# Kernel tuning notes

Measured on AMD Instinct MI355X. Metric: run time of the kernel, lower is better.

Reference implementation:

```python
import jax, jax.numpy as jnp
import numpy as np

B, N, C, H = 2, 4096, 512, 8
D = C // H          # head dim = 64
EPS = 1e-5          # nn.LayerNorm default eps


def _layernorm(x, gamma, beta):
    m = jnp.mean(x, axis=-1, keepdims=True)
    v = jnp.var(x, axis=-1, keepdims=True)
    return (x - m) * jax.lax.rsqrt(v + EPS) * gamma + beta


def setup_inputs() -> dict:
    key = jax.random.key(0)
    k_x, k_w = jax.random.split(key, 2)
    return {
        "x": jax.random.normal(k_x, (B, N, C), dtype=jnp.float32),
        "w_qkv": jax.random.normal(k_w, (C, 3 * C), dtype=jnp.float32) * 0.02,
        "b_qkv": jnp.zeros((3 * C,), dtype=jnp.float32),
        "g_pre": jnp.ones((C,), dtype=jnp.float32),
        "beta_pre": jnp.zeros((C,), dtype=jnp.float32),
        "g_post": jnp.ones((C,), dtype=jnp.float32),
        "beta_post": jnp.zeros((C,), dtype=jnp.float32),
    }


def reference(x, w_qkv, b_qkv, g_pre, beta_pre, g_post, beta_post):
    b, n, c = x.shape
    xn = _layernorm(x, g_pre, beta_pre)                       # pre_norm (x is reassigned in source)
    qkv = (xn @ w_qkv + b_qkv).reshape(b, n, 3, H, D)
    qkv = jnp.transpose(qkv, (2, 0, 3, 1, 4))                 # [3, B, H, N, D]
    q, k, v = qkv[0], qkv[1], qkv[2]
    scale = D ** (-0.5)
    attn = jnp.einsum('bhnd,bhmd->bhnm', q, k) * scale        # [B, H, N, N]
    soft = jax.nn.softmax(attn, axis=-1)
    val = jnp.einsum('bhnm,bhmd->bhnd', soft, v)              # [B, H, N, D]
    val = jnp.transpose(val, (0, 2, 1, 3)).reshape(b, n, c)   # [B, N, C]
    val = _layernorm(val, g_post, beta_post)                  # post_norm
    return xn + val                                            # residual uses pre-normed x (faithful)
```

## Files before the change

### kernel.cpp

```cpp
#include <hip/hip_runtime.h>

#define BB   2
#define NN   4096
#define CC   512
#define HH   8
#define DD   64
#define MR   8192
#define NC3  1536
#define PS   4194304
#define SPLK 1408

typedef __attribute__((ext_vector_type(8))) short short8;
typedef __attribute__((ext_vector_type(4))) short short4v;
typedef __attribute__((ext_vector_type(4))) float floatx4;

#if __has_builtin(__builtin_amdgcn_mfma_f32_16x16x16_bf16_1k)
#define MFMA16(a, b, c) __builtin_amdgcn_mfma_f32_16x16x16_bf16_1k(a, b, c, 0, 0, 0)
#elif __has_builtin(__builtin_amdgcn_mfma_f32_16x16x16_bf16)
#define MFMA16(a, b, c) __builtin_amdgcn_mfma_f32_16x16x16_bf16(a, b, c, 0, 0, 0)
#else
__device__ inline floatx4 mfma16_asm(short4v a, short4v b, floatx4 c) {
  asm volatile("v_mfma_f32_16x16x16_bf16 %0, %1, %2, %0" : "+v"(c) : "v"(a), "v"(b));
  return c;
}
#define MFMA16(a, b, c) mfma16_asm(a, b, c)
#endif

__device__ inline unsigned short f2bf(float f) {
  unsigned int u = __float_as_uint(f);
  u = (u + 0x7fffu + ((u >> 16) & 1u)) >> 16;
  return (unsigned short)u;
}

__device__ inline unsigned int pack_bf2(float a, float b) {
  unsigned int ua = __float_as_uint(a) + 0x8000u;
  unsigned int ub = __float_as_uint(b) + 0x8000u;
  return (ub & 0xffff0000u) | (ua >> 16);
}

__device__ inline short4v pack_bf4(float a, float b, float c, float d) {
  union { unsigned int u[2]; short4v v; } t;
  t.u[0] = pack_bf2(a, b);
  t.u[1] = pack_bf2(c, d);
  return t.v;
}

__device__ inline floatx4 fzero4() { floatx4 z = {0.f, 0.f, 0.f, 0.f}; return z; }

__device__ inline void async_cp16(const void* g, void* l) {
  __builtin_amdgcn_global_load_lds(
      (const __attribute__((address_space(1))) unsigned int*)g,
      (__attribute__((address_space(3))) unsigned int*)l, 16, 0, 0);
}

__global__ __launch_bounds__(256) void convert_w_kernel(
    const float* __restrict__ w, unsigned short* __restrict__ wt) {
  __shared__ short T[64][68];
  int bn = blockIdx.x;
  int bk = blockIdx.y;
  int tid = threadIdx.x;
  for (int p = 0; p < 4; p++) {
    int k = p * 16 + (tid >> 4);
    int n4 = (tid & 15) * 4;
    float4 v = *(const float4*)&w[(size_t)(bk * 64 + k) * NC3 + bn * 64 + n4];
    T[n4 + 0][k] = (short)f2bf(v.x);
    T[n4 + 1][k] = (short)f2bf(v.y);
    T[n4 + 2][k] = (short)f2bf(v.z);
    T[n4 + 3][k] = (short)f2bf(v.w);
  }
  __syncthreads();
  for (int p = 0; p < 2; p++) {
    int n = p * 32 + (tid >> 3);
    int k8 = (tid & 7) * 8;
    uint4 v = *(uint4*)&T[n][k8];
    *(uint4*)&wt[(size_t)(bn * 64 + n) * 512 + bk * 64 + k8] = v;
  }
}

__global__ __launch_bounds__(256) void pre_ln_kernel(
    const float* __restrict__ x, const float* __restrict__ g,
    const float* __restrict__ be, unsigned short* __restrict__ xnb) {
  int wv = threadIdx.x >> 6, lane = threadIdx.x & 63;
  int row = blockIdx.x * 4 + wv;
  const float4* xr = (const float4*)(x + (size_t)row * CC);
  float4 v0 = xr[lane];
  float4 v1 = xr[64 + lane];
  float s  = (v0.x + v0.y) + (v0.z + v0.w) + (v1.x + v1.y) + (v1.z + v1.w);
  float sq = (v0.x * v0.x + v0.y * v0.y) + (v0.z * v0.z + v0.w * v0.w) +
             (v1.x * v1.x + v1.y * v1.y) + (v1.z * v1.z + v1.w * v1.w);
  for (int off = 1; off < 64; off <<= 1) {
    s  += __shfl_xor(s,  off, 64);
    sq += __shfl_xor(sq, off, 64);
  }
  float mean = s * (1.0f / CC);
  float var  = sq * (1.0f / CC) - mean * mean;
  float rstd = rsqrtf(var + 1e-5f);
  const float4* gg = (const float4*)g;
  const float4* bb = (const float4*)be;
  float4 g0 = gg[lane], g1 = gg[64 + lane];
  float4 b0 = bb[lane], b1 = bb[64 + lane];
  float4 o0, o1;
  o0.x = (v0.x - mean) * rstd * g0.x + b0.x;
  o0.y = (v0.y - mean) * rstd * g0.y + b0.y;
  o0.z = (v0.z - mean) * rstd * g0.z + b0.z;
  o0.w = (v0.w - mean) * rstd * g0.w + b0.w;
  o1.x = (v1.x - mean) * rstd * g1.x + b1.x;
  o1.y = (v1.y - mean) * rstd * g1.y + b1.y;
  o1.z = (v1.z - mean) * rstd * g1.z + b1.z;
  o1.w = (v1.w - mean) * rstd * g1.w + b1.w;
  size_t base = (size_t)row * CC;
  uint2 u0, u1;
  u0.x = pack_bf2(o0.x, o0.y); u0.y = pack_bf2(o0.z, o0.w);
  u1.x = pack_bf2(o1.x, o1.y); u1.y = pack_bf2(o1.z, o1.w);
  *(uint2*)&xnb[base + 4 * lane] = u0;
  *(uint2*)&xnb[base + 256 + 4 * lane] = u1;
}

#define QSCALE 0.180336879f

__global__ __launch_bounds__(256) void qkv_gemm_kernel(
    const unsigned short* __restrict__ xnb, const unsigned short* __restrict__ wt,
    const float* __restrict__ bias, unsigned short* __restrict__ qkvb) {
  __shared__ __align__(16) char smem[65536];
  short (*Asb[2])[64];
  short (*Bsb[2])[64];
  Asb[0] = (short (*)[64])smem;
  Bsb[0] = (short (*)[64])(smem + 16384);
  Asb[1] = (short (*)[64])(smem + 32768);
  Bsb[1] = (short (*)[64])(smem + 49152);
  short (*T)[136] = (short (*)[136])smem;

  int tn = blockIdx.x;
  int tm = blockIdx.y;
  int tid = threadIdx.x;
  int wv = tid >> 6, lane = tid & 63;
  int quad = lane >> 4, l16 = lane & 15;
  int wm = wv >> 1, wn = wv & 1;
  int l7 = l16 & 7;

  int kr = lane >> 3;
  int kg = (lane & 7) ^ kr;

  floatx4 acc[4][4];
  for (int i = 0; i < 4; i++) for (int j = 0; j < 4; j++) acc[i][j] = fzero4();

  for (int i = 0; i < 4; i++) {
    int rb = i * 32 + wv * 8;
    async_cp16(&xnb[(size_t)(tm * 128 + rb + kr) * 512 + kg * 8], &Asb[0][rb][0]);
    async_cp16(&wt [(size_t)(tn * 128 + rb + kr) * 512 + kg * 8], &Bsb[0][rb][0]);
  }

  for (int it = 0; it < 8; it++) {
    __syncthreads();
    short (*As)[64] = Asb[it & 1];
    short (*Bs)[64] = Bsb[it & 1];
    if (it < 7) {
      int kn = (it + 1) * 64;
      short (*An)[64] = Asb[(it + 1) & 1];
      short (*Bn)[64] = Bsb[(it + 1) & 1];
      for (int i = 0; i < 4; i++) {
        int rb = i * 32 + wv * 8;
        async_cp16(&xnb[(size_t)(tm * 128 + rb + kr) * 512 + kn + kg * 8], &An[rb][0]);
        async_cp16(&wt [(size_t)(tn * 128 + rb + kr) * 512 + kn + kg * 8], &Bn[rb][0]);
      }
    }
    for (int kk = 0; kk < 2; kk++) {
      short8 a[4], b[4];
      for (int mt = 0; mt < 4; mt++)
        a[mt] = *(const short8*)&As[wm * 64 + mt * 16 + l16][((kk * 4 + quad) ^ l7) * 8];
      for (int nt = 0; nt < 4; nt++)
        b[nt] = *(const short8*)&Bs[wn * 64 + nt * 16 + l16][((kk * 4 + quad) ^ l7) * 8];
      for (int mt = 0; mt < 4; mt++)
        for (int nt = 0; nt < 4; nt++)
          acc[mt][nt] = __builtin_amdgcn_mfma_f32_16x16x32_bf16(a[mt], b[nt], acc[mt][nt], 0, 0, 0);
    }
  }
  __syncthreads();

  int part = tn >> 2;
  int b = tm >> 5;
  int tloc = (tm & 31) * 128;

  if (part < 2) {
    for (int nt = 0; nt < 4; nt++) {
      int coll = wn * 64 + nt * 16 + l16;
      float bv = bias[tn * 128 + coll];
      for (int mt = 0; mt < 4; mt++) {
        int rowb = wm * 64 + mt * 16 + quad * 4;
        for (int r = 0; r < 4; r++) {
          float v = acc[mt][nt][r] + bv;
          if (part == 0) v *= QSCALE;
          T[rowb + r][coll] = (short)f2bf(v);
        }
      }
    }
    __syncthreads();
    int h0 = (tn & 3) * 2;
    for (int it = 0; it < 8; it++) {
      int row = it * 16 + (tid >> 4);
      int l = tid & 15;
      uint4 vv = *(uint4*)&T[row][l * 8];
      int h = h0 + (l >> 3), d = (l & 7) * 8;
      size_t idx = (size_t)part * PS +
                   ((size_t)((b * 8 + h) * 4096 + tloc + row)) * 64 + d;
      *(uint4*)&qkvb[idx] = vv;
    }
  } else {
    for (int nt = 0; nt < 4; nt++) {
      int coll = wn * 64 + nt * 16 + l16;
      float bv = bias[tn * 128 + coll];
      for (int mt = 0; mt < 4; mt++) {
        int rowb = wm * 64 + mt * 16 + quad * 4;
        uint2 w;
        w.x = pack_bf2(acc[mt][nt][0] + bv, acc[mt][nt][1] + bv);
        w.y = pack_bf2(acc[mt][nt][2] + bv, acc[mt][nt][3] + bv);
        *(uint2*)&T[coll][rowb] = w;
      }
    }
    __syncthreads();
    for (int it = 0; it < 8; it++) {
      int vrow = it * 16 + (tid >> 4);
      int l = tid & 15;
      uint4 vv = *(uint4*)&T[vrow][l * 8];
      int gj = tn * 128 + vrow;
      int h = (gj >> 6) & 7, d = gj & 63;
      size_t idx = 2 * (size_t)PS +
                   ((size_t)((b * 8 + h) * 64 + d)) * 4096 + tloc + l * 8;
      *(uint4*)&qkvb[idx] = vv;
    }
  }
}

#define SMEM_ATT (16384 + 32768)

__global__ __launch_bounds__(256, 3) void attn_kernel(
    const unsigned short* __restrict__ qkvb, unsigned short* __restrict__ valp,
    float* __restrict__ lsum) {
  __shared__ __align__(16) char smem[SMEM_ATT];
  short (*Ks)[64]   = (short (*)[64])smem;
  short (*Vt0)[128] = (short (*)[128])(smem + 16384);
  short (*Vt1)[128] = (short (*)[128])(smem + 32768);
  float (*slab)[68] = (float (*)[68])smem;

  int bh = blockIdx.y;
  int qb = blockIdx.x * 128;
  int ksp = blockIdx.z;
  int kts = (ksp < 2) ? 11 : 10;
  int tid = threadIdx.x;
  int wv = tid >> 6, lane = tid & 63, quad = lane >> 4, l16 = lane & 15;
  int l7 = l16 & 7;
  const unsigned short* Qg = qkvb + (size_t)bh * NN * DD;
  const unsigned short* Kg = qkvb + (size_t)PS + (size_t)bh * NN * DD +
                             (size_t)ksp * SPLK * DD;
  const unsigned short* Vg = qkvb + 2 * (size_t)PS + (size_t)bh * DD * NN +
                             (size_t)ksp * SPLK;

  int kr = lane >> 3;
  int kg = (lane & 7) ^ kr;
  int vr = lane >> 4;
  int vgr = (lane & 15) ^ ((wv * 4 + vr) & 15);

  for (int i = 0; i < 4; i++) {
    int rb = i * 32 + wv * 8;
    async_cp16(&Qg[(size_t)(qb + rb + kr) * 64 + kg * 8], &Ks[rb][0]);
  }
  __syncthreads();
  short8 qf[2][2];
  for (int g = 0; g < 2; g++)
    for (int kk = 0; kk < 2; kk++)
      qf[g][kk] = *(const short8*)&Ks[wv * 32 + g * 16 + l16][((kk * 4 + quad) ^ l7) * 8];
  __syncthreads();

  for (int i = 0; i < 4; i++) {
    int rb = i * 32 + wv * 8;
    async_cp16(&Kg[(size_t)(rb + kr) * 64 + kg * 8], &Ks[rb][0]);
  }
  for (int i = 0; i < 4; i++) {
    int rb = i * 16 + wv * 4;
    async_cp16(&Vg[(size_t)(rb + vr) * NN + vgr * 8], &Vt0[rb][0]);
  }

  floatx4 o[2][4];
  for (int g = 0; g < 2; g++) for (int dt = 0; dt < 4; dt++) o[g][dt] = fzero4();
  float ls[2] = {0.0f, 0.0f};

  for (int kt = 0; kt < kts; kt++) {
    __syncthreads();
    short (*Vc)[128] = (kt & 1) ? Vt1 : Vt0;
    short (*Vn)[128] = (kt & 1) ? Vt0 : Vt1;
    if (kt + 1 < kts) {
      int kn = (kt + 1) * 128;
      for (int i = 0; i < 4; i++) {
        int rb = i * 16 + wv * 4;
        async_cp16(&Vg[(size_t)(rb + vr) * NN + kn + vgr * 8], &Vn[rb][0]);
      }
    }

    floatx4 s[2][8];
    for (int nt = 0; nt < 8; nt++) {
      short8 kf0 = *(const short8*)&Ks[nt * 16 + l16][((quad) ^ l7) * 8];
      short8 kf1 = *(const short8*)&Ks[nt * 16 + l16][((4 + quad) ^ l7) * 8];
      floatx4 s0 = fzero4(), s1 = fzero4();
      s0 = __builtin_amdgcn_mfma_f32_16x16x32_bf16(kf0, qf[0][0], s0, 0, 0, 0);
      s0 = __builtin_amdgcn_mfma_f32_16x16x32_bf16(kf1, qf[0][1], s0, 0, 0, 0);
      s1 = __builtin_amdgcn_mfma_f32_16x16x32_bf16(kf0, qf[1][0], s1, 0, 0, 0);
      s1 = __builtin_amdgcn_mfma_f32_16x16x32_bf16(kf1, qf[1][1], s1, 0, 0, 0);
      s[0][nt] = s0;
      s[1][nt] = s1;
    }
    __syncthreads();
    if (kt + 1 < kts) {
      int kn = (kt + 1) * 128;
      for (int i = 0; i < 4; i++) {
        int rb = i * 32 + wv * 8;
        async_cp16(&Kg[(size_t)(kn + rb + kr) * 64 + kg * 8], &Ks[rb][0]);
      }
    }

    for (int nt = 0; nt < 8; nt++) {
      float p00 = __builtin_amdgcn_exp2f(s[0][nt][0]);
      float p01 = __builtin_amdgcn_exp2f(s[0][nt][1]);
      float p02 = __builtin_amdgcn_exp2f(s[0][nt][2]);
      float p03 = __builtin_amdgcn_exp2f(s[0][nt][3]);
      float p10 = __builtin_amdgcn_exp2f(s[1][nt][0]);
      float p11 = __builtin_amdgcn_exp2f(s[1][nt][1]);
      float p12 = __builtin_amdgcn_exp2f(s[1][nt][2]);
      float p13 = __builtin_amdgcn_exp2f(s[1][nt][3]);
      ls[0] += (p00 + p01) + (p02 + p03);
      ls[1] += (p10 + p11) + (p12 + p13);
      short4v pa0 = pack_bf4(p00, p01, p02, p03);
      short4v pa1 = pack_bf4(p10, p11, p12, p13);
      for (int dt = 0; dt < 4; dt++) {
        short4v vb = *(const short4v*)&Vc[dt * 16 + l16]
            [(((nt * 2 + (quad >> 1)) ^ l16) * 8) + (quad & 1) * 4];
        o[0][dt] = MFMA16(vb, pa0, o[0][dt]);
        o[1][dt] = MFMA16(vb, pa1, o[1][dt]);
      }
    }
  }

  for (int g = 0; g < 2; g++) {
    ls[g] += __shfl_xor(ls[g], 16, 64);
    ls[g] += __shfl_xor(ls[g], 32, 64);
  }
  float* lrow = lsum + (size_t)(ksp * 16 + bh) * 4096 + qb;
  if (lane < 16) {
    lrow[wv * 32 + l16] = ls[0];
    lrow[wv * 32 + 16 + l16] = ls[1];
  }

  __syncthreads();
  for (int g = 0; g < 2; g++) {
    int q = wv * 32 + g * 16 + l16;
    for (int dt = 0; dt < 4; dt++)
      for (int r = 0; r < 4; r++)
        slab[q][dt * 16 + quad * 4 + r] = o[g][dt][r];
  }
  __syncthreads();
  int b = bh >> 3, h = bh & 7;
  unsigned short* myval = valp + (size_t)ksp * MR * CC;
  for (int it = 0; it < 4; it++) {
    int row = it * 32 + (tid >> 3);
    int col8 = (tid & 7) * 8;
    float4 a = *(float4*)&slab[row][col8];
    float4 c = *(float4*)&slab[row][col8 + 4];
    uint4 u;
    u.x = pack_bf2(a.x, a.y);  u.y = pack_bf2(a.z, a.w);
    u.z = pack_bf2(c.x, c.y);  u.w = pack_bf2(c.z, c.w);
    *(uint4*)&myval[((size_t)(b * 4096 + qb + row)) * 512 + h * 64 + col8] = u;
  }
}

__global__ __launch_bounds__(256) void post_ln_kernel(
    const unsigned short* __restrict__ valp, const float* __restrict__ lsum,
    const unsigned short* __restrict__ xnb,
    const float* __restrict__ g, const float* __restrict__ be,
    float* __restrict__ out) {
  int wv = threadIdx.x >> 6, lane = threadIdx.x & 63;
  int row = blockIdx.x * 4 + wv;
  int b = row >> 12, q = row & 4095;
  int h = lane >> 3;
  float acc[8];
  for (int j = 0; j < 8; j++) acc[j] = 0.0f;
  float lt = 0.0f;
  for (int sp = 0; sp < 3; sp++) {
    uint4 u = *(const uint4*)&valp[((size_t)sp * MR + row) * CC + lane * 8];
    acc[0] += __uint_as_float(u.x << 16);
    acc[1] += __uint_as_float(u.x & 0xffff0000u);
    acc[2] += __uint_as_float(u.y << 16);
    acc[3] += __uint_as_float(u.y & 0xffff0000u);
    acc[4] += __uint_as_float(u.z << 16);
    acc[5] += __uint_as_float(u.z & 0xffff0000u);
    acc[6] += __uint_as_float(u.w << 16);
    acc[7] += __uint_as_float(u.w & 0xffff0000u);
    lt += lsum[(size_t)(sp * 16 + b * 8 + h) * 4096 + q];
  }
  float inv = 1.0f / lt;
  float s = 0.0f, sq = 0.0f;
  for (int j = 0; j < 8; j++) {
    acc[j] *= inv;
    s += acc[j];
    sq += acc[j] * acc[j];
  }
  for (int off = 1; off < 64; off <<= 1) {
    s  += __shfl_xor(s,  off, 64);
    sq += __shfl_xor(sq, off, 64);
  }
  float mean = s * (1.0f / CC);
  float var  = sq * (1.0f / CC) - mean * mean;
  float rstd = rsqrtf(var + 1e-5f);
  float4 g0 = ((const float4*)g)[lane * 2];
  float4 g1 = ((const float4*)g)[lane * 2 + 1];
  float4 b0 = ((const float4*)be)[lane * 2];
  float4 b1 = ((const float4*)be)[lane * 2 + 1];
  size_t base = (size_t)row * CC + lane * 8;
  uint4 xr = *(const uint4*)&xnb[base];
  float r[8];
  r[0] = __uint_as_float(xr.x << 16);  r[1] = __uint_as_float(xr.x & 0xffff0000u);
  r[2] = __uint_as_float(xr.y << 16);  r[3] = __uint_as_float(xr.y & 0xffff0000u);
  r[4] = __uint_as_float(xr.z << 16);  r[5] = __uint_as_float(xr.z & 0xffff0000u);
  r[6] = __uint_as_float(xr.w << 16);  r[7] = __uint_as_float(xr.w & 0xffff0000u);
  float4 o0, o1;
  o0.x = (acc[0] - mean) * rstd * g0.x + b0.x + r[0];
  o0.y = (acc[1] - mean) * rstd * g0.y + b0.y + r[1];
  o0.z = (acc[2] - mean) * rstd * g0.z + b0.z + r[2];
  o0.w = (acc[3] - mean) * rstd * g0.w + b0.w + r[3];
  o1.x = (acc[4] - mean) * rstd * g1.x + b1.x + r[4];
  o1.y = (acc[5] - mean) * rstd * g1.y + b1.y + r[5];
  o1.z = (acc[6] - mean) * rstd * g1.z + b1.z + r[6];
  o1.w = (acc[7] - mean) * rstd * g1.w + b1.w + r[7];
  *(float4*)&out[base] = o0;
  *(float4*)&out[base + 4] = o1;
}

extern "C" void kernel_launch(void* const* d_in, const int* in_sizes, int n_in,
                              void* d_out, int out_size, void* d_ws, size_t ws_size,
                              hipStream_t stream) {
  const float* x       = (const float*)d_in[0];
  const float* w_qkv   = (const float*)d_in[1];
  const float* b_qkv   = (const float*)d_in[2];
  const float* g_pre   = (const float*)d_in[3];
  const float* be_pre  = (const float*)d_in[4];
  const float* g_post  = (const float*)d_in[5];
  const float* be_post = (const float*)d_in[6];
  float* out = (float*)d_out;

  unsigned short* val  = (unsigned short*)d_ws;
  float* lsum = (float*)(val + 3 * (size_t)MR * CC);
  unsigned short* xnb  = (unsigned short*)(lsum + 3 * 16 * 4096);
  unsigned short* qkvb = xnb + 4194304;
  unsigned short* wt   = qkvb + 3 * (size_t)PS;

  convert_w_kernel<<<dim3(24, 8), 256, 0, stream>>>(w_qkv, wt);
  pre_ln_kernel<<<2048, 256, 0, stream>>>(x, g_pre, be_pre, xnb);
  qkv_gemm_kernel<<<dim3(12, 64), 256, 0, stream>>>(xnb, wt, b_qkv, qkvb);
  attn_kernel<<<dim3(32, 16, 3), 256, 0, stream>>>(qkvb, val, lsum);
  post_ln_kernel<<<2048, 256, 0, stream>>>(val, lsum, xnb, g_post, be_post, out);
}
```

Measured before the change: 201.6 us.

## Drop double buffering in GEMM and attention, use two-way key split

Both the QKV GEMM and the attention kernel replace double-buffered async loads with a single LDS buffer, loaded synchronously and fenced by two barriers per iteration. This shrinks shared memory to about 34 KB so more blocks fit per CU (launch bounds raised to 3 and 4). The attention key dimension is now split in two halves of 2048 instead of three uneven chunks, which cuts the grid and the partial sums post-LN must combine. The cost is that load latency is no longer overlapped with MFMA work inside a block; the design relies on extra resident blocks to hide it.

```diff
diff --git a/kernel.cpp b/kernel.cpp
--- a/kernel.cpp
+++ b/kernel.cpp
@@ -8,7 +8,6 @@
 #define MR   8192
 #define NC3  1536
 #define PS   4194304
-#define SPLK 1408
 
 typedef __attribute__((ext_vector_type(8))) short short8;
 typedef __attribute__((ext_vector_type(4))) short short4v;
@@ -118,16 +117,12 @@
 
 #define QSCALE 0.180336879f
 
-__global__ __launch_bounds__(256) void qkv_gemm_kernel(
+__global__ __launch_bounds__(256, 3) void qkv_gemm_kernel(
     const unsigned short* __restrict__ xnb, const unsigned short* __restrict__ wt,
     const float* __restrict__ bias, unsigned short* __restrict__ qkvb) {
-  __shared__ __align__(16) char smem[65536];
-  short (*Asb[2])[64];
-  short (*Bsb[2])[64];
-  Asb[0] = (short (*)[64])smem;
-  Bsb[0] = (short (*)[64])(smem + 16384);
-  Asb[1] = (short (*)[64])(smem + 32768);
-  Bsb[1] = (short (*)[64])(smem + 49152);
+  __shared__ __align__(16) char smem[34816];
+  short (*As)[64] = (short (*)[64])smem;
+  short (*Bs)[64] = (short (*)[64])(smem + 16384);
   short (*T)[136] = (short (*)[136])smem;
 
   int tn = blockIdx.x;
@@ -144,26 +139,15 @@
   floatx4 acc[4][4];
   for (int i = 0; i < 4; i++) for (int j = 0; j < 4; j++) acc[i][j] = fzero4();
 
-  for (int i = 0; i < 4; i++) {
-    int rb = i * 32 + wv * 8;
-    async_cp16(&xnb[(size_t)(tm * 128 + rb + kr) * 512 + kg * 8], &Asb[0][rb][0]);
-    async_cp16(&wt [(size_t)(tn * 128 + rb + kr) * 512 + kg * 8], &Bsb[0][rb][0]);
-  }
-
   for (int it = 0; it < 8; it++) {
     __syncthreads();
-    short (*As)[64] = Asb[it & 1];
-    short (*Bs)[64] = Bsb[it & 1];
-    if (it < 7) {
-      int kn = (it + 1) * 64;
-      short (*An)[64] = Asb[(it + 1) & 1];
-      short (*Bn)[64] = Bsb[(it + 1) & 1];
-      for (int i = 0; i < 4; i++) {
-        int rb = i * 32 + wv * 8;
-        async_cp16(&xnb[(size_t)(tm * 128 + rb + kr) * 512 + kn + kg * 8], &An[rb][0]);
-        async_cp16(&wt [(size_t)(tn * 128 + rb + kr) * 512 + kn + kg * 8], &Bn[rb][0]);
-      }
-    }
+    int k0 = it * 64;
+    for (int i = 0; i < 4; i++) {
+      int rb = i * 32 + wv * 8;
+      async_cp16(&xnb[(size_t)(tm * 128 + rb + kr) * 512 + k0 + kg * 8], &As[rb][0]);
+      async_cp16(&wt [(size_t)(tn * 128 + rb + kr) * 512 + k0 + kg * 8], &Bs[rb][0]);
+    }
+    __syncthreads();
     for (int kk = 0; kk < 2; kk++) {
       short8 a[4], b[4];
       for (int mt = 0; mt < 4; mt++)
@@ -231,29 +215,27 @@
   }
 }
 
-#define SMEM_ATT (16384 + 32768)
-
-__global__ __launch_bounds__(256, 3) void attn_kernel(
+#define SMEM_ATT 34816
+
+__global__ __launch_bounds__(256, 4) void attn_kernel(
     const unsigned short* __restrict__ qkvb, unsigned short* __restrict__ valp,
     float* __restrict__ lsum) {
   __shared__ __align__(16) char smem[SMEM_ATT];
   short (*Ks)[64]   = (short (*)[64])smem;
-  short (*Vt0)[128] = (short (*)[128])(smem + 16384);
-  short (*Vt1)[128] = (short (*)[128])(smem + 32768);
+  short (*Vt)[128]  = (short (*)[128])(smem + 16384);
   float (*slab)[68] = (float (*)[68])smem;
 
   int bh = blockIdx.y;
   int qb = blockIdx.x * 128;
   int ksp = blockIdx.z;
-  int kts = (ksp < 2) ? 11 : 10;
   int tid = threadIdx.x;
   int wv = tid >> 6, lane = tid & 63, quad = lane >> 4, l16 = lane & 15;
   int l7 = l16 & 7;
   const unsigned short* Qg = qkvb + (size_t)bh * NN * DD;
   const unsigned short* Kg = qkvb + (size_t)PS + (size_t)bh * NN * DD +
-                             (size_t)ksp * SPLK * DD;
+                             (size_t)ksp * 2048 * DD;
   const unsigned short* Vg = qkvb + 2 * (size_t)PS + (size_t)bh * DD * NN +
-                             (size_t)ksp * SPLK;
+                             (size_t)ksp * 2048;
 
   int kr = lane >> 3;
   int kg = (lane & 7) ^ kr;
@@ -269,32 +251,23 @@
   for (int g = 0; g < 2; g++)
     for (int kk = 0; kk < 2; kk++)
       qf[g][kk] = *(const short8*)&Ks[wv * 32 + g * 16 + l16][((kk * 4 + quad) ^ l7) * 8];
-  __syncthreads();
-
-  for (int i = 0; i < 4; i++) {
-    int rb = i * 32 + wv * 8;
-    async_cp16(&Kg[(size_t)(rb + kr) * 64 + kg * 8], &Ks[rb][0]);
-  }
-  for (int i = 0; i < 4; i++) {
-    int rb = i * 16 + wv * 4;
-    async_cp16(&Vg[(size_t)(rb + vr) * NN + vgr * 8], &Vt0[rb][0]);
-  }
 
   floatx4 o[2][4];
   for (int g = 0; g < 2; g++) for (int dt = 0; dt < 4; dt++) o[g][dt] = fzero4();
   float ls[2] = {0.0f, 0.0f};
 
-  for (int kt = 0; kt < kts; kt++) {
-    __syncthreads();
-    short (*Vc)[128] = (kt & 1) ? Vt1 : Vt0;
-    short (*Vn)[128] = (kt & 1) ? Vt0 : Vt1;
-    if (kt + 1 < kts) {
-      int kn = (kt + 1) * 128;
-      for (int i = 0; i < 4; i++) {
-        int rb = i * 16 + wv * 4;
-        async_cp16(&Vg[(size_t)(rb + vr) * NN + kn + vgr * 8], &Vn[rb][0]);
-      }
-    }
+  for (int kt = 0; kt < 16; kt++) {
+    __syncthreads();
+    int kn = kt * 128;
+    for (int i = 0; i < 4; i++) {
+      int rb = i * 32 + wv * 8;
+      async_cp16(&Kg[(size_t)(kn + rb + kr) * 64 + kg * 8], &Ks[rb][0]);
+    }
+    for (int i = 0; i < 4; i++) {
+      int rb = i * 16 + wv * 4;
+      async_cp16(&Vg[(size_t)(rb + vr) * NN + kn + vgr * 8], &Vt[rb][0]);
+    }
+    __syncthreads();
 
     floatx4 s[2][8];
     for (int nt = 0; nt < 8; nt++) {
@@ -307,14 +280,6 @@
       s1 = __builtin_amdgcn_mfma_f32_16x16x32_bf16(kf1, qf[1][1], s1, 0, 0, 0);
       s[0][nt] = s0;
       s[1][nt] = s1;
-    }
-    __syncthreads();
-    if (kt + 1 < kts) {
-      int kn = (kt + 1) * 128;
-      for (int i = 0; i < 4; i++) {
-        int rb = i * 32 + wv * 8;
-        async_cp16(&Kg[(size_t)(kn + rb + kr) * 64 + kg * 8], &Ks[rb][0]);
-      }
     }
 
     for (int nt = 0; nt < 8; nt++) {
@@ -331,7 +296,7 @@
       short4v pa0 = pack_bf4(p00, p01, p02, p03);
       short4v pa1 = pack_bf4(p10, p11, p12, p13);
       for (int dt = 0; dt < 4; dt++) {
-        short4v vb = *(const short4v*)&Vc[dt * 16 + l16]
+        short4v vb = *(const short4v*)&Vt[dt * 16 + l16]
             [(((nt * 2 + (quad >> 1)) ^ l16) * 8) + (quad & 1) * 4];
         o[0][dt] = MFMA16(vb, pa0, o[0][dt]);
         o[1][dt] = MFMA16(vb, pa1, o[1][dt]);
@@ -383,7 +348,7 @@
   float acc[8];
   for (int j = 0; j < 8; j++) acc[j] = 0.0f;
   float lt = 0.0f;
-  for (int sp = 0; sp < 3; sp++) {
+  for (int sp = 0; sp < 2; sp++) {
     uint4 u = *(const uint4*)&valp[((size_t)sp * MR + row) * CC + lane * 8];
     acc[0] += __uint_as_float(u.x << 16);
     acc[1] += __uint_as_float(u.x & 0xffff0000u);
@@ -446,14 +411,14 @@
   float* out = (float*)d_out;
 
   unsigned short* val  = (unsigned short*)d_ws;
-  float* lsum = (float*)(val + 3 * (size_t)MR * CC);
-  unsigned short* xnb  = (unsigned short*)(lsum + 3 * 16 * 4096);
+  float* lsum = (float*)(val + 2 * (size_t)MR * CC);
+  unsigned short* xnb  = (unsigned short*)(lsum + 2 * 16 * 4096);
   unsigned short* qkvb = xnb + 4194304;
   unsigned short* wt   = qkvb + 3 * (size_t)PS;
 
   convert_w_kernel<<<dim3(24, 8), 256, 0, stream>>>(w_qkv, wt);
   pre_ln_kernel<<<2048, 256, 0, stream>>>(x, g_pre, be_pre, xnb);
   qkv_gemm_kernel<<<dim3(12, 64), 256, 0, stream>>>(xnb, wt, b_qkv, qkvb);
-  attn_kernel<<<dim3(32, 16, 3), 256, 0, stream>>>(qkvb, val, lsum);
+  attn_kernel<<<dim3(32, 16, 2), 256, 0, stream>>>(qkvb, val, lsum);
   post_ln_kernel<<<2048, 256, 0, stream>>>(val, lsum, xnb, g_post, be_post, out);
 }
```

Measured after the change: 255.6 us. 26.8% more time.
